# Kernel tuning notes

Hardware: AMD Instinct MI355X
Metric: run time of the kernel (lower is better)

## Reference

```python
import jax, jax.numpy as jnp
import numpy as np

DIM = 768
HEADS = 16
DIM_HEAD = DIM // HEADS
SCALE = DIM_HEAD ** -0.5


def setup_inputs() -> dict:
    key = jax.random.key(0)
    k1, k2, k3, k4 = jax.random.split(key, 4)
    B, N = 8, 1024
    x = jax.random.normal(k1, (B, N, DIM), dtype=jnp.float32)
    # nn.Linear(dim, 3*dim, bias=False): stored so that qkv = x @ Wqkv
    Wqkv = jax.random.normal(k2, (DIM, 3 * DIM), dtype=jnp.float32) * (DIM ** -0.5)
    Wo = jax.random.normal(k3, (DIM, DIM), dtype=jnp.float32) * (DIM ** -0.5)
    bo = jax.random.normal(k4, (DIM,), dtype=jnp.float32) * 0.01
    return {"x": x, "Wqkv": Wqkv, "Wo": Wo, "bo": bo}


def reference(x, Wqkv, Wo, bo):
    B, N, _ = x.shape
    qkv = x @ Wqkv                                   # [B, N, 3*dim]
    # Faithful to torch: qkv.view(3, B, h, N, dim_head) — raw memory reshape
    qkv = jnp.reshape(qkv, (3, B, HEADS, N, DIM_HEAD))
    q, k, v = qkv[0], qkv[1], qkv[2]                 # each [B, h, N, dh]
    attn = jnp.einsum('bhnd,bhmd->bhnm', q, k) * SCALE   # [B, h, N, N]
    weight = jax.nn.softmax(attn, axis=-1)
    context = jnp.einsum('bhnm,bhmd->bhnd', weight, v)   # [B, h, N, dh]
    # Faithful to torch: context.view(B, -1, dim) — raw memory reshape
    concat = jnp.reshape(context, (B, N, DIM))
    return concat @ Wo + bo                          # dropout is identity at eval
```

## Files before the change

kernel.cpp:

```cpp
#include <hip/hip_runtime.h>
#include <hip/hip_bf16.h>

typedef __bf16 bf16x8 __attribute__((ext_vector_type(8)));
typedef __bf16 bf16x4 __attribute__((ext_vector_type(4)));
typedef float  f32x4  __attribute__((ext_vector_type(4)));

#define C2LOG 0.20823509f

__device__ __forceinline__ void gload_lds16(const __bf16* g, __bf16* l) {
    __builtin_amdgcn_global_load_lds(
        (const __attribute__((address_space(1))) void*)g,
        (__attribute__((address_space(3))) void*)l,
        16, 0, 0);
}

__global__ __launch_bounds__(256)
void prepass_kernel(const float* __restrict__ x, const float* __restrict__ Wqkv,
                    const float* __restrict__ Wo, __bf16* __restrict__ Xbf,
                    __bf16* __restrict__ WqkvT, __bf16* __restrict__ WoT) {
    __shared__ float tile[32][33];
    const int bx = blockIdx.x, t = threadIdx.x;
    if (bx < 6144) {
        const int i = (bx * 256 + t) * 4;
        float4 v = *(const float4*)&x[i];
        bf16x4 o;
        o[0] = (__bf16)v.x; o[1] = (__bf16)v.y; o[2] = (__bf16)v.z; o[3] = (__bf16)v.w;
        *(bf16x4*)&Xbf[i] = o;
        return;
    }
    const float* in; __bf16* out; int R, C, bxx;
    if (bx < 6144 + 1728) { bxx = bx - 6144; in = Wqkv; out = WqkvT; R = 768; C = 2304;
        const int c0 = (bxx % 72) * 32, r0 = (bxx / 72) * 32;
        const int tx = t & 31, ty = t >> 5;
#pragma unroll
        for (int i = 0; i < 4; ++i)
            tile[ty + i * 8][tx] = in[(size_t)(r0 + ty + i * 8) * C + c0 + tx];
        __syncthreads();
#pragma unroll
        for (int i = 0; i < 4; ++i)
            out[(size_t)(c0 + ty + i * 8) * R + r0 + tx] = (__bf16)tile[tx][ty + i * 8];
    } else { bxx = bx - 6144 - 1728; in = Wo; out = WoT; R = 768; C = 768;
        const int c0 = (bxx % 24) * 32, r0 = (bxx / 24) * 32;
        const int tx = t & 31, ty = t >> 5;
#pragma unroll
        for (int i = 0; i < 4; ++i)
            tile[ty + i * 8][tx] = in[(size_t)(r0 + ty + i * 8) * C + c0 + tx];
        __syncthreads();
#pragma unroll
        for (int i = 0; i < 4; ++i)
            out[(size_t)(c0 + ty + i * 8) * R + r0 + tx] = (__bf16)tile[tx][ty + i * 8];
    }
}

__global__ __launch_bounds__(512, 2)
void gemm_bt_kernel(const __bf16* __restrict__ A, const __bf16* __restrict__ B,
                    __bf16* __restrict__ C, int M, int N, int K) {
    __shared__ __bf16 sA[256 * 64];
    __shared__ __bf16 sB[128 * 64];

    const int m0 = blockIdx.y * 256;
    const int n0 = blockIdx.x * 128;
    const int t = threadIdx.x;
    const int w = t >> 6, lane = t & 63;
    const int quad = lane >> 4, l15 = lane & 15;
    const int wm = w >> 1, wn = w & 1;

    int sRow[4], sKc[4];
#pragma unroll
    for (int b = 0; b < 4; ++b) {
        const int L = b * 512 + t;
        sRow[b] = L >> 3;
        sKc[b] = (L & 7) ^ (sRow[b] & 7);
    }

    f32x4 acc[4][4] = {};

    for (int k0 = 0; k0 < K; k0 += 64) {
#pragma unroll
        for (int b = 0; b < 4; ++b)
            gload_lds16(A + (size_t)(m0 + sRow[b]) * K + k0 + sKc[b] * 8,
                        &sA[(b * 512 + w * 64) * 8]);
#pragma unroll
        for (int b = 0; b < 2; ++b)
            gload_lds16(B + (size_t)(n0 + sRow[b]) * K + k0 + sKc[b] * 8,
                        &sB[(b * 512 + w * 64) * 8]);
        __syncthreads();

#pragma unroll
        for (int ks = 0; ks < 2; ++ks) {
            bf16x8 aF[4], bF[4];
            const int slot = ((ks * 4 + quad) ^ (l15 & 7)) * 8;
#pragma unroll
            for (int mt = 0; mt < 4; ++mt)
                aF[mt] = *(const bf16x8*)&sA[(wm * 64 + mt * 16 + l15) * 64 + slot];
#pragma unroll
            for (int nt = 0; nt < 4; ++nt)
                bF[nt] = *(const bf16x8*)&sB[(wn * 64 + nt * 16 + l15) * 64 + slot];
#pragma unroll
            for (int mt = 0; mt < 4; ++mt)
#pragma unroll
                for (int nt = 0; nt < 4; ++nt)
                    acc[mt][nt] = __builtin_amdgcn_mfma_f32_16x16x32_bf16(aF[mt], bF[nt], acc[mt][nt], 0, 0, 0);
        }
        __syncthreads();
    }

#pragma unroll
    for (int nt = 0; nt < 4; ++nt) {
        const int col = n0 + wn * 64 + nt * 16 + l15;
#pragma unroll
        for (int mt = 0; mt < 4; ++mt)
#pragma unroll
            for (int r = 0; r < 4; ++r) {
                const int row = m0 + wm * 64 + mt * 16 + quad * 4 + r;
                C[(size_t)row * N + col] = (__bf16)acc[mt][nt][r];
            }
    }
}

__global__ __launch_bounds__(256, 4)
void gemm_bt64_kernel(const __bf16* __restrict__ A, const __bf16* __restrict__ B,
                      float* __restrict__ C, const float* __restrict__ bias,
                      int M, int N, int K) {
    __shared__ __bf16 sA[128 * 64];
    __shared__ __bf16 sB[64 * 64];

    const int m0 = blockIdx.y * 128;
    const int n0 = blockIdx.x * 64;
    const int t = threadIdx.x;
    const int w = t >> 6, lane = t & 63;
    const int quad = lane >> 4, l15 = lane & 15;

    int sRow[4], sKc[4];
#pragma unroll
    for (int b = 0; b < 4; ++b) {
        const int L = b * 256 + t;
        sRow[b] = L >> 3;
        sKc[b] = (L & 7) ^ (sRow[b] & 7);
    }

    f32x4 acc[2][4] = {};

    for (int k0 = 0; k0 < K; k0 += 64) {
#pragma unroll
        for (int b = 0; b < 4; ++b)
            gload_lds16(A + (size_t)(m0 + sRow[b]) * K + k0 + sKc[b] * 8,
                        &sA[(b * 256 + w * 64) * 8]);
#pragma unroll
        for (int b = 0; b < 2; ++b)
            gload_lds16(B + (size_t)(n0 + sRow[b]) * K + k0 + sKc[b] * 8,
                        &sB[(b * 256 + w * 64) * 8]);
        __syncthreads();

#pragma unroll
        for (int ks = 0; ks < 2; ++ks) {
            bf16x8 aF[2], bF[4];
            const int slot = ((ks * 4 + quad) ^ (l15 & 7)) * 8;
#pragma unroll
            for (int mt = 0; mt < 2; ++mt)
                aF[mt] = *(const bf16x8*)&sA[(w * 32 + mt * 16 + l15) * 64 + slot];
#pragma unroll
            for (int nt = 0; nt < 4; ++nt)
                bF[nt] = *(const bf16x8*)&sB[(nt * 16 + l15) * 64 + slot];
#pragma unroll
            for (int mt = 0; mt < 2; ++mt)
#pragma unroll
                for (int nt = 0; nt < 4; ++nt)
                    acc[mt][nt] = __builtin_amdgcn_mfma_f32_16x16x32_bf16(aF[mt], bF[nt], acc[mt][nt], 0, 0, 0);
        }
        __syncthreads();
    }

#pragma unroll
    for (int nt = 0; nt < 4; ++nt) {
        const int col = n0 + nt * 16 + l15;
        const float bv = bias[col];
#pragma unroll
        for (int mt = 0; mt < 2; ++mt)
#pragma unroll
            for (int r = 0; r < 4; ++r) {
                const int row = m0 + w * 32 + mt * 16 + quad * 4 + r;
                C[(size_t)row * N + col] = acc[mt][nt][r] + bv;
            }
    }
}

#define VT_STRIDE 132
#define P_STRIDE  132

__global__ __launch_bounds__(256, 2)
void attn_kernel(const __bf16* __restrict__ Y1, __bf16* __restrict__ Ctx) {
    __shared__ __bf16 Kl[128 * 64];
    __shared__ __bf16 Vt[48 * VT_STRIDE];
    __shared__ __bf16 Pl[128 * P_STRIDE];

    const int bx = blockIdx.x;
    const int bh = bx & 127, qt = bx >> 7;
    const int t = threadIdx.x, w = t >> 6, lane = t & 63;
    const int quad = lane >> 4, l15 = lane & 15;

    const size_t qBase = (size_t)bh * 49152;
    const size_t kBase = 6291456 + qBase;
    const size_t vBase = 12582912 + qBase;

    bf16x8 qf0[2], qf1[2];
#pragma unroll
    for (int mt = 0; mt < 2; ++mt) {
        const int row = qt * 128 + w * 32 + mt * 16 + l15;
        bf16x8 a = *(const bf16x8*)(Y1 + qBase + (size_t)row * 48 + quad * 8);
#pragma unroll
        for (int j = 0; j < 8; ++j) a[j] = (__bf16)((float)a[j] * C2LOG);
        qf0[mt] = a;
        if (quad < 2) {
            bf16x8 b = *(const bf16x8*)(Y1 + qBase + (size_t)row * 48 + 32 + quad * 8);
#pragma unroll
            for (int j = 0; j < 8; ++j) b[j] = (__bf16)((float)b[j] * C2LOG);
            qf1[mt] = b;
        } else qf1[mt] = bf16x8{};
    }

    int kr[4], kd[4];
#pragma unroll
    for (int b = 0; b < 4; ++b) {
        const int L = t + b * 256;
        kr[b] = L >> 3;
        kd[b] = L & 7;
    }
    int vkp[6], vdb[6], vkk[6];
#pragma unroll
    for (int c = 0; c < 6; ++c) {
        const int u = t + c * 256;
        vkp[c] = u & 127;
        vdb[c] = (u >> 7) * 4;
        vkk[c] = (vkp[c] >> 3) + ((vkp[c] & 7) << 4);
    }

    bf16x8 kreg[4];
#pragma unroll
    for (int b = 0; b < 4; ++b)
        kreg[b] = *(const bf16x8*)(Y1 + kBase + (size_t)kr[b] * 48 + kd[b] * 8);
    bf16x4 vreg[6];
#pragma unroll
    for (int c = 0; c < 6; ++c)
        vreg[c] = *(const bf16x4*)(Y1 + vBase + (size_t)vkk[c] * 48 + vdb[c]);

    f32x4 o[2][3] = {};
    float l_lane[2][4] = {};

    for (int it = 0; it < 8; ++it) {
        __syncthreads();

#pragma unroll
        for (int b = 0; b < 4; ++b)
            *(bf16x8*)&Kl[kr[b] * 64 + ((kd[b] ^ (kr[b] & 7)) << 3)] = kreg[b];
#pragma unroll
        for (int c = 0; c < 6; ++c)
#pragma unroll
            for (int j = 0; j < 4; ++j)
                Vt[(vdb[c] + j) * VT_STRIDE + vkp[c]] = vreg[c][j];

        if (it < 7) {
            const int kv1 = (it + 1) * 128;
#pragma unroll
            for (int b = 0; b < 4; ++b)
                kreg[b] = *(const bf16x8*)(Y1 + kBase + (size_t)(kv1 + kr[b]) * 48 + kd[b] * 8);
#pragma unroll
            for (int c = 0; c < 6; ++c)
                vreg[c] = *(const bf16x4*)(Y1 + vBase + (size_t)(kv1 + vkk[c]) * 48 + vdb[c]);
        }

        __syncthreads();

        f32x4 s[2][8];
#pragma unroll
        for (int nt = 0; nt < 8; ++nt) {
            const int krow = nt * 16 + l15;
            const int base = krow * 64;
            bf16x8 kf0 = *(const bf16x8*)&Kl[base + ((quad ^ (krow & 7)) << 3)];
            bf16x8 kf1 = *(const bf16x8*)&Kl[base + (((4 + quad) ^ (krow & 7)) << 3)];
#pragma unroll
            for (int mt = 0; mt < 2; ++mt) {
                f32x4 z = {};
                z = __builtin_amdgcn_mfma_f32_16x16x32_bf16(qf0[mt], kf0, z, 0, 0, 0);
                s[mt][nt] = __builtin_amdgcn_mfma_f32_16x16x32_bf16(qf1[mt], kf1, z, 0, 0, 0);
            }
        }

#pragma unroll
        for (int mt = 0; mt < 2; ++mt)
#pragma unroll
            for (int r = 0; r < 4; ++r) {
                bf16x8 pk;
                float ls = 0.f;
#pragma unroll
                for (int nt = 0; nt < 8; ++nt) {
                    float p = __builtin_amdgcn_exp2f(s[mt][nt][r]);
                    ls += p;
                    pk[nt] = (__bf16)p;
                }
                l_lane[mt][r] += ls;
                *(bf16x8*)&Pl[(w * 32 + mt * 16 + quad * 4 + r) * P_STRIDE + l15 * 8] = pk;
            }

        bf16x8 pa[2][4];
#pragma unroll
        for (int mt = 0; mt < 2; ++mt)
#pragma unroll
            for (int ks = 0; ks < 4; ++ks)
                pa[mt][ks] = *(const bf16x8*)&Pl[(w * 32 + mt * 16 + l15) * P_STRIDE + ks * 32 + quad * 8];
#pragma unroll
        for (int nd = 0; nd < 3; ++nd)
#pragma unroll
            for (int ks = 0; ks < 4; ++ks) {
                bf16x8 vb = *(const bf16x8*)&Vt[(nd * 16 + l15) * VT_STRIDE + ks * 32 + quad * 8];
#pragma unroll
                for (int mt = 0; mt < 2; ++mt)
                    o[mt][nd] = __builtin_amdgcn_mfma_f32_16x16x32_bf16(pa[mt][ks], vb, o[mt][nd], 0, 0, 0);
            }
    }

    float inv[2][4];
#pragma unroll
    for (int mt = 0; mt < 2; ++mt)
#pragma unroll
        for (int r = 0; r < 4; ++r) {
            float ls = l_lane[mt][r];
#pragma unroll
            for (int off = 1; off < 16; off <<= 1)
                ls += __shfl_xor(ls, off);
            inv[mt][r] = __builtin_amdgcn_rcpf(ls);
        }

    __syncthreads();
    __bf16* Ob = Vt;
#pragma unroll
    for (int mt = 0; mt < 2; ++mt)
#pragma unroll
        for (int nd = 0; nd < 3; ++nd) {
            const int d = nd * 16 + l15;
#pragma unroll
            for (int r = 0; r < 4; ++r)
                Ob[(w * 32 + mt * 16 + quad * 4 + r) * 48 + d] = (__bf16)(o[mt][nd][r] * inv[mt][r]);
        }
    __syncthreads();
    __bf16* dst = Ctx + qBase + (size_t)qt * 128 * 48;
#pragma unroll
    for (int c = 0; c < 3; ++c)
        *(bf16x8*)(dst + (t + c * 256) * 8) = *(const bf16x8*)&Ob[(t + c * 256) * 8];
}

extern "C" void kernel_launch(void* const* d_in, const int* in_sizes, int n_in,
                              void* d_out, int out_size, void* d_ws, size_t ws_size,
                              hipStream_t stream) {
    const float* x    = (const float*)d_in[0];
    const float* Wqkv = (const float*)d_in[1];
    const float* Wo   = (const float*)d_in[2];
    const float* bo   = (const float*)d_in[3];
    float* out = (float*)d_out;

    char* ws = (char*)d_ws;
    __bf16* Xbf    = (__bf16*)(ws + 0);
    __bf16* WqkvT  = (__bf16*)(ws + 12582912);
    __bf16* WoT    = (__bf16*)(ws + 16121856);
    __bf16* Y1     = (__bf16*)(ws + 17301504);
    __bf16* Ctx    = (__bf16*)(ws + 55050240);

    prepass_kernel<<<8448, 256, 0, stream>>>(x, Wqkv, Wo, Xbf, WqkvT, WoT);

    gemm_bt_kernel<<<dim3(18, 32), 512, 0, stream>>>(Xbf, WqkvT, Y1, 8192, 2304, 768);

    attn_kernel<<<1024, 256, 0, stream>>>(Y1, Ctx);

    gemm_bt64_kernel<<<dim3(12, 64), 256, 0, stream>>>(Ctx, WoT, out, bo, 8192, 768, 768);
}
```

Measured before the change: 202.7 us.

## Load K fragments directly from global memory and drop K LDS staging

The attention kernel no longer stages K tiles through shared memory. Each wave now reads its K MFMA fragments straight from global memory (relying on L1/L2 reuse), and exp/sum/pack is fused right after each score MFMA instead of buffering all scores. Removing the K buffer, the K prefetch registers and the score array frees LDS and registers, so launch bounds are raised to allow 3 blocks per CU. The risk is higher global/L2 traffic and exposed load latency for K, since it is no longer software-prefetched a tile ahead.

```diff
diff --git a/kernel.cpp b/kernel.cpp
--- a/kernel.cpp
+++ b/kernel.cpp
@@ -188,9 +188,8 @@
 #define VT_STRIDE 132
 #define P_STRIDE  132
 
-__global__ __launch_bounds__(256, 2)
+__global__ __launch_bounds__(256, 3)
 void attn_kernel(const __bf16* __restrict__ Y1, __bf16* __restrict__ Ctx) {
-    __shared__ __bf16 Kl[128 * 64];
     __shared__ __bf16 Vt[48 * VT_STRIDE];
     __shared__ __bf16 Pl[128 * P_STRIDE];
 
@@ -219,13 +218,6 @@
         } else qf1[mt] = bf16x8{};
     }
 
-    int kr[4], kd[4];
-#pragma unroll
-    for (int b = 0; b < 4; ++b) {
-        const int L = t + b * 256;
-        kr[b] = L >> 3;
-        kd[b] = L & 7;
-    }
     int vkp[6], vdb[6], vkk[6];
 #pragma unroll
     for (int c = 0; c < 6; ++c) {
@@ -234,11 +226,6 @@
         vdb[c] = (u >> 7) * 4;
         vkk[c] = (vkp[c] >> 3) + ((vkp[c] & 7) << 4);
     }
-
-    bf16x8 kreg[4];
-#pragma unroll
-    for (int b = 0; b < 4; ++b)
-        kreg[b] = *(const bf16x8*)(Y1 + kBase + (size_t)kr[b] * 48 + kd[b] * 8);
     bf16x4 vreg[6];
 #pragma unroll
     for (int c = 0; c < 6; ++c)
@@ -248,11 +235,9 @@
     float l_lane[2][4] = {};
 
     for (int it = 0; it < 8; ++it) {
-        __syncthreads();
-
-#pragma unroll
-        for (int b = 0; b < 4; ++b)
-            *(bf16x8*)&Kl[kr[b] * 64 + ((kd[b] ^ (kr[b] & 7)) << 3)] = kreg[b];
+        const int kv0 = it * 128;
+        __syncthreads();
+
 #pragma unroll
         for (int c = 0; c < 6; ++c)
 #pragma unroll
@@ -260,29 +245,31 @@
                 Vt[(vdb[c] + j) * VT_STRIDE + vkp[c]] = vreg[c][j];
 
         if (it < 7) {
-            const int kv1 = (it + 1) * 128;
-#pragma unroll
-            for (int b = 0; b < 4; ++b)
-                kreg[b] = *(const bf16x8*)(Y1 + kBase + (size_t)(kv1 + kr[b]) * 48 + kd[b] * 8);
+            const int kv1 = kv0 + 128;
 #pragma unroll
             for (int c = 0; c < 6; ++c)
                 vreg[c] = *(const bf16x4*)(Y1 + vBase + (size_t)(kv1 + vkk[c]) * 48 + vdb[c]);
         }
 
-        __syncthreads();
-
-        f32x4 s[2][8];
+        bf16x8 pk[2][4];
+        float ls[2][4] = {};
 #pragma unroll
         for (int nt = 0; nt < 8; ++nt) {
-            const int krow = nt * 16 + l15;
-            const int base = krow * 64;
-            bf16x8 kf0 = *(const bf16x8*)&Kl[base + ((quad ^ (krow & 7)) << 3)];
-            bf16x8 kf1 = *(const bf16x8*)&Kl[base + (((4 + quad) ^ (krow & 7)) << 3)];
+            const int krow = kv0 + nt * 16 + l15;
+            const __bf16* kp = Y1 + kBase + (size_t)krow * 48 + quad * 8;
+            bf16x8 kf0 = *(const bf16x8*)kp;
+            bf16x8 kf1 = *(const bf16x8*)(kp + 32);
 #pragma unroll
             for (int mt = 0; mt < 2; ++mt) {
                 f32x4 z = {};
                 z = __builtin_amdgcn_mfma_f32_16x16x32_bf16(qf0[mt], kf0, z, 0, 0, 0);
-                s[mt][nt] = __builtin_amdgcn_mfma_f32_16x16x32_bf16(qf1[mt], kf1, z, 0, 0, 0);
+                f32x4 sv = __builtin_amdgcn_mfma_f32_16x16x32_bf16(qf1[mt], kf1, z, 0, 0, 0);
+#pragma unroll
+                for (int r = 0; r < 4; ++r) {
+                    float p = __builtin_amdgcn_exp2f(sv[r]);
+                    ls[mt][r] += p;
+                    pk[mt][r][nt] = (__bf16)p;
+                }
             }
         }
 
@@ -290,17 +277,11 @@
         for (int mt = 0; mt < 2; ++mt)
 #pragma unroll
             for (int r = 0; r < 4; ++r) {
-                bf16x8 pk;
-                float ls = 0.f;
-#pragma unroll
-                for (int nt = 0; nt < 8; ++nt) {
-                    float p = __builtin_amdgcn_exp2f(s[mt][nt][r]);
-                    ls += p;
-                    pk[nt] = (__bf16)p;
-                }
-                l_lane[mt][r] += ls;
-                *(bf16x8*)&Pl[(w * 32 + mt * 16 + quad * 4 + r) * P_STRIDE + l15 * 8] = pk;
-            }
+                l_lane[mt][r] += ls[mt][r];
+                *(bf16x8*)&Pl[(w * 32 + mt * 16 + quad * 4 + r) * P_STRIDE + l15 * 8] = pk[mt][r];
+            }
+
+        __syncthreads();
 
         bf16x8 pa[2][4];
 #pragma unroll
```

New measurement: 234.8 us. 1.16x slower.
